# Kernel tuning notes

Hardware: AMD Instinct MI355X
Metric: run time of the kernel (lower is better)

The kernel has to match this reference:

```python
import jax, jax.numpy as jnp
import numpy as np

B, S, E, H, D = 16, 1024, 768, 12, 64  # batch, seq, n_embd, n_head, head_dim
F = 4 * E
EPS = 1e-5


def layernorm(x, g, b):
    mu = jnp.mean(x, axis=-1, keepdims=True)
    var = jnp.mean((x - mu) ** 2, axis=-1, keepdims=True)
    return (x - mu) * jax.lax.rsqrt(var + EPS) * g + b


def setup_inputs() -> dict:
    key = jax.random.key(0)
    ks = jax.random.split(key, 12)
    w = lambda k, shape: jax.random.normal(k, shape, dtype=jnp.float32) * 0.02
    return {
        "x": jax.random.normal(ks[0], (B, S, E), dtype=jnp.float32),
        # per-head q/k/v projections stacked over heads: [H, E, D]
        "Wq": w(ks[1], (H, E, D)), "bq": jnp.zeros((H, D), jnp.float32),
        "Wk": w(ks[2], (H, E, D)), "bk": jnp.zeros((H, D), jnp.float32),
        "Wv": w(ks[3], (H, E, D)), "bv": jnp.zeros((H, D), jnp.float32),
        "Wp": w(ks[4], (E, E)), "bp": jnp.zeros((E,), jnp.float32),
        "ln1_g": jnp.ones((E,), jnp.float32), "ln1_b": jnp.zeros((E,), jnp.float32),
        "ln2_g": jnp.ones((E,), jnp.float32), "ln2_b": jnp.zeros((E,), jnp.float32),
        "W1": w(ks[5], (E, F)), "b1": jnp.zeros((F,), jnp.float32),
        "W2": w(ks[6], (F, E)), "b2": jnp.zeros((E,), jnp.float32),
        "lnf_g": jnp.ones((E,), jnp.float32), "lnf_b": jnp.zeros((E,), jnp.float32),
    }


def reference(x, Wq, bq, Wk, bk, Wv, bv, Wp, bp,
              ln1_g, ln1_b, ln2_g, ln2_b, W1, b1, W2, b2, lnf_g, lnf_b):
    # --- multi-head causal attention (batched over heads, same math as the
    # per-head loop in the original) ---
    h = layernorm(x, ln1_g, ln1_b)
    q = jnp.einsum('bse,hed->bhsd', h, Wq) + bq[None, :, None, :]
    k = jnp.einsum('bse,hed->bhsd', h, Wk) + bk[None, :, None, :]
    v = jnp.einsum('bse,hed->bhsd', h, Wv) + bv[None, :, None, :]
    scores = jnp.einsum('bhsd,bhtd->bhst', q, k)
    causal = jnp.tril(jnp.ones((S, S), dtype=bool))
    # original: mask with -inf, then divide by sqrt(head_dim), then softmax
    scores = jnp.where(causal, scores, -jnp.inf) / np.sqrt(D).astype(np.float32)
    attn = jax.nn.softmax(scores, axis=-1)
    o = jnp.einsum('bhst,bhtd->bhsd', attn, v)
    o = o.transpose(0, 2, 1, 3).reshape(B, S, E)  # concat heads
    x = x + (o @ Wp + bp)
    # --- FFN with post-net LayerNorm (as in the original FeedForward) ---
    h2 = layernorm(x, ln2_g, ln2_b)
    f = jax.nn.gelu(h2 @ W1 + b1, approximate=False) @ W2 + b2
    f = layernorm(f, lnf_g, lnf_b)
    return x + f
```

## Files before the change

kernel.cpp:

```cpp
#include <hip/hip_runtime.h>
#include <math.h>

typedef unsigned short u16;
typedef __attribute__((ext_vector_type(8))) short s16x8;
typedef __attribute__((ext_vector_type(4))) float f32x4;

#define NB 16
#define NS 1024
#define NE 768
#define NH 12
#define ND 64
#define NF 3072
#define NBS (NB*NS)
#define NBH (NB*NH)

__device__ __forceinline__ u16 f2bf(float f){
  unsigned u = __float_as_uint(f);
  unsigned r = (u + 0x7fffu + ((u >> 16) & 1u)) >> 16;
  return (u16)r;
}

__device__ __forceinline__ void gload16(const void* g, void* l){
  __builtin_amdgcn_global_load_lds((const __attribute__((address_space(1))) void*)g,
                                   (__attribute__((address_space(3))) void*)l, 16, 0, 0);
}

__global__ __launch_bounds__(256) void pack_t(const float* __restrict__ W,
                                              u16* __restrict__ Wt, int N, int K){
  __shared__ u16 tile[64*72];
  const int tid = threadIdx.x;
  const int n0 = blockIdx.x*64, k0 = blockIdx.y*64;
  #pragma unroll
  for (int it = 0; it < 4; ++it){
    int c = it*256 + tid;
    int row = c >> 4, col = (c & 15) * 4;
    float4 v = *(const float4*)(W + (size_t)(k0+row)*N + n0 + col);
    tile[row*72+col+0] = f2bf(v.x); tile[row*72+col+1] = f2bf(v.y);
    tile[row*72+col+2] = f2bf(v.z); tile[row*72+col+3] = f2bf(v.w);
  }
  __syncthreads();
  #pragma unroll
  for (int it = 0; it < 2; ++it){
    int c = it*256 + tid;
    int nr = c >> 3, kc = (c & 7) * 8;
    s16x8 val;
    #pragma unroll
    for (int j = 0; j < 8; ++j) val[j] = tile[(kc+j)*72 + nr];
    *(s16x8*)(Wt + (size_t)(n0+nr)*K + k0 + kc) = val;
  }
}

__global__ __launch_bounds__(256) void pack_qkv(const float* __restrict__ Wq,
    const float* __restrict__ Wk, const float* __restrict__ Wv,
    const float* __restrict__ bq, const float* __restrict__ bk,
    const float* __restrict__ bv, u16* __restrict__ Wt, float* __restrict__ bias){
  __shared__ u16 tile[64*72];
  const int tid = threadIdx.x;
  const int n0 = blockIdx.x*64, e0 = blockIdx.y*64;
  const int p = n0 / NE, rr = n0 % NE, h = rr >> 6;
  const float* Wsrc = (p==0) ? Wq : ((p==1) ? Wk : Wv);
  #pragma unroll
  for (int it = 0; it < 4; ++it){
    int c = it*256 + tid;
    int row = c >> 4, col = (c & 15) * 4;
    float4 v = *(const float4*)(Wsrc + ((size_t)h*NE + e0 + row)*ND + col);
    tile[row*72+col+0] = f2bf(v.x); tile[row*72+col+1] = f2bf(v.y);
    tile[row*72+col+2] = f2bf(v.z); tile[row*72+col+3] = f2bf(v.w);
  }
  __syncthreads();
  #pragma unroll
  for (int it = 0; it < 2; ++it){
    int c = it*256 + tid;
    int dr = c >> 3, ec = (c & 7) * 8;
    s16x8 val;
    #pragma unroll
    for (int j = 0; j < 8; ++j) val[j] = tile[(ec+j)*72 + dr];
    *(s16x8*)(Wt + (size_t)(n0+dr)*NE + e0 + ec) = val;
  }
  if (e0 == 0 && tid < 64){
    const float* bsrc = (p==0) ? bq : ((p==1) ? bk : bv);
    bias[n0 + tid] = bsrc[rr + tid];
  }
}

__global__ __launch_bounds__(256) void ln_bf16(const float* __restrict__ x,
    const float* __restrict__ g, const float* __restrict__ b, u16* __restrict__ out){
  __shared__ float red[4];
  const int row = blockIdx.x, tid = threadIdx.x;
  const float* xr = x + (size_t)row*NE;
  float v0 = xr[tid], v1 = xr[tid+256], v2 = xr[tid+512];
  float s = v0 + v1 + v2;
  #pragma unroll
  for (int off = 32; off > 0; off >>= 1) s += __shfl_down(s, off);
  if ((tid & 63) == 0) red[tid >> 6] = s;
  __syncthreads();
  float mu = (red[0]+red[1]+red[2]+red[3]) * (1.f/NE);
  float d0 = v0-mu, d1 = v1-mu, d2 = v2-mu;
  float q = d0*d0 + d1*d1 + d2*d2;
  #pragma unroll
  for (int off = 32; off > 0; off >>= 1) q += __shfl_down(q, off);
  __syncthreads();
  if ((tid & 63) == 0) red[tid >> 6] = q;
  __syncthreads();
  float rs = rsqrtf((red[0]+red[1]+red[2]+red[3]) * (1.f/NE) + 1e-5f);
  u16* orow = out + (size_t)row*NE;
  orow[tid]     = f2bf(d0*rs*g[tid]     + b[tid]);
  orow[tid+256] = f2bf(d1*rs*g[tid+256] + b[tid+256]);
  orow[tid+512] = f2bf(d2*rs*g[tid+512] + b[tid+512]);
}

__global__ __launch_bounds__(256) void ln_add_out(const float* __restrict__ f2,
    const float* __restrict__ g, const float* __restrict__ b, float* __restrict__ x1){
  __shared__ float red[4];
  const int row = blockIdx.x, tid = threadIdx.x;
  const float* xr = f2 + (size_t)row*NE;
  float v0 = xr[tid], v1 = xr[tid+256], v2 = xr[tid+512];
  float s = v0 + v1 + v2;
  #pragma unroll
  for (int off = 32; off > 0; off >>= 1) s += __shfl_down(s, off);
  if ((tid & 63) == 0) red[tid >> 6] = s;
  __syncthreads();
  float mu = (red[0]+red[1]+red[2]+red[3]) * (1.f/NE);
  float d0 = v0-mu, d1 = v1-mu, d2 = v2-mu;
  float q = d0*d0 + d1*d1 + d2*d2;
  #pragma unroll
  for (int off = 32; off > 0; off >>= 1) q += __shfl_down(q, off);
  __syncthreads();
  if ((tid & 63) == 0) red[tid >> 6] = q;
  __syncthreads();
  float rs = rsqrtf((red[0]+red[1]+red[2]+red[3]) * (1.f/NE) + 1e-5f);
  float* orow = x1 + (size_t)row*NE;
  orow[tid]     += d0*rs*g[tid]     + b[tid];
  orow[tid+256] += d1*rs*g[tid+256] + b[tid+256];
  orow[tid+512] += d2*rs*g[tid+512] + b[tid+512];
}

template<int EPI>
__global__ __launch_bounds__(256, 2)
void gemm_bt(const u16* __restrict__ A, const u16* __restrict__ Bt,
             const float* __restrict__ bias, const float* __restrict__ resid,
             float* __restrict__ outF, u16* __restrict__ outU,
             u16* __restrict__ oq, u16* __restrict__ ok, u16* __restrict__ ov,
             int M, int N, int K)
{
  __shared__ u16 As[128*32];
  __shared__ u16 Bs[128*32];
  const int tid = threadIdx.x;
  const int lane = tid & 63, wv = tid >> 6;
  const int wm = wv >> 1, wn = wv & 1;
  const int r = lane & 15, g4 = lane >> 4;
  const int m0 = blockIdx.y*128, n0 = blockIdx.x*128;

  f32x4 acc[4][4] = {};

  for (int kt = 0; kt < K; kt += 32) {
    __syncthreads();
    #pragma unroll
    for (int it = 0; it < 2; ++it) {
      int c = it*256 + tid;
      int row = c >> 2, kc = (c & 3) << 3;
      gload16(A  + (size_t)(m0+row)*K + kt + kc, As + (size_t)(it*256 + wv*64)*8);
      gload16(Bt + (size_t)(n0+row)*K + kt + kc, Bs + (size_t)(it*256 + wv*64)*8);
    }
    __syncthreads();
    s16x8 aF[4], bF[4];
    #pragma unroll
    for (int mi = 0; mi < 4; ++mi)
      aF[mi] = *(const s16x8*)(As + (wm*64 + mi*16 + r)*32 + g4*8);
    #pragma unroll
    for (int ni = 0; ni < 4; ++ni)
      bF[ni] = *(const s16x8*)(Bs + (wn*64 + ni*16 + r)*32 + g4*8);
    #pragma unroll
    for (int mi = 0; mi < 4; ++mi)
      #pragma unroll
      for (int ni = 0; ni < 4; ++ni)
        acc[mi][ni] = __builtin_amdgcn_mfma_f32_16x16x32_bf16(aF[mi], bF[ni], acc[mi][ni], 0, 0, 0);
  }

  const int colb = n0 + wn*64, rowb = m0 + wm*64;
  #pragma unroll
  for (int mi = 0; mi < 4; ++mi) {
    #pragma unroll
    for (int ni = 0; ni < 4; ++ni) {
      const int col = colb + ni*16 + r;
      const float bv = bias[col];
      #pragma unroll
      for (int i = 0; i < 4; ++i) {
        const int row = rowb + mi*16 + g4*4 + i;
        float v = acc[mi][ni][i] + bv;
        if (EPI == 0) {
          int p = col / NE, rr2 = col % NE;
          int hh = rr2 >> 6, d = rr2 & 63;
          int bb = row >> 10, ss = row & (NS-1);
          size_t idx = (((size_t)(bb*NH + hh))*NS + ss)*ND + d;
          u16 val = f2bf(v);
          if (p == 0) oq[idx] = val;
          else if (p == 1) ok[idx] = val;
          else ov[idx] = val;
        } else if (EPI == 1) {
          size_t idx = (size_t)row*NE + col;
          outF[idx] = resid[idx] + v;
        } else if (EPI == 2) {
          float ge = 0.5f * v * (1.0f + erff(v * 0.70710678118654752f));
          outU[(size_t)row*NF + col] = f2bf(ge);
        } else {
          outF[(size_t)row*NE + col] = v;
        }
      }
    }
  }
}

__global__ __launch_bounds__(256) void transpose_v(const u16* __restrict__ v,
                                                   u16* __restrict__ vT){
  __shared__ u16 tile[64*80];
  const int tid = threadIdx.x;
  const int t0 = blockIdx.x*64, bh = blockIdx.y;
  const u16* src = v + ((size_t)bh*NS + t0)*ND;
  #pragma unroll
  for (int it = 0; it < 2; ++it){
    int c = it*256 + tid;
    int row = c >> 3, col = (c & 7) * 8;
    *(s16x8*)(tile + row*80 + col) = *(const s16x8*)(src + (size_t)row*ND + col);
  }
  __syncthreads();
  u16* dst = vT + (size_t)bh*ND*NS + t0;
  #pragma unroll
  for (int it = 0; it < 2; ++it){
    int c = it*256 + tid;
    int d = c >> 3, tc = (c & 7) * 8;
    s16x8 val;
    #pragma unroll
    for (int j = 0; j < 8; ++j) val[j] = tile[(tc+j)*80 + d];
    *(s16x8*)(dst + (size_t)d*NS + tc) = val;
  }
}

__global__ __launch_bounds__(256, 2)
void attn(const u16* __restrict__ q, const u16* __restrict__ k,
          const u16* __restrict__ vT, u16* __restrict__ o)
{
  __shared__ u16 Ks[64*80];
  __shared__ u16 Vs[64*80];
  __shared__ u16 Ps[64*80];
  const int tid = threadIdx.x, lane = tid & 63, w = tid >> 6;
  const int r = lane & 15, g4 = lane >> 4;
  const int qt = blockIdx.x, bh = blockIdx.y;
  const int qs0 = qt*64;
  const int bb = bh / NH, hh = bh % NH;

  const u16* qrow = q + ((size_t)bh*NS + qs0 + w*16 + r)*ND;
  s16x8 qf0 = *(const s16x8*)(qrow + g4*8);
  s16x8 qf1 = *(const s16x8*)(qrow + 32 + g4*8);

  f32x4 oacc[4] = {};
  float mrow[4], lrow[4];
  #pragma unroll
  for (int i = 0; i < 4; ++i){ mrow[i] = -INFINITY; lrow[i] = 0.f; }

  const u16* kbase = k  + (size_t)bh*NS*ND;
  const u16* vbase = vT + (size_t)bh*ND*NS;

  for (int kt0 = 0; kt0 <= qs0; kt0 += 64) {
    __syncthreads();
    #pragma unroll
    for (int it = 0; it < 2; ++it) {
      int c = it*256 + tid;
      int rowi = c >> 3, coli = (c & 7) * 8;
      *(s16x8*)(Ks + rowi*80 + coli) = *(const s16x8*)(kbase + (size_t)(kt0+rowi)*ND + coli);
      *(s16x8*)(Vs + rowi*80 + coli) = *(const s16x8*)(vbase + (size_t)rowi*NS + kt0 + coli);
    }
    __syncthreads();

    f32x4 sc[4];
    #pragma unroll
    for (int ni = 0; ni < 4; ++ni) {
      s16x8 kf0 = *(const s16x8*)(Ks + (ni*16+r)*80 + g4*8);
      s16x8 kf1 = *(const s16x8*)(Ks + (ni*16+r)*80 + 32 + g4*8);
      f32x4 t = {};
      t = __builtin_amdgcn_mfma_f32_16x16x32_bf16(qf0, kf0, t, 0, 0, 0);
      t = __builtin_amdgcn_mfma_f32_16x16x32_bf16(qf1, kf1, t, 0, 0, 0);
      sc[ni] = t;
    }
    const bool diag = (kt0 == qs0);
    float mx[4];
    #pragma unroll
    for (int i = 0; i < 4; ++i) mx[i] = -INFINITY;
    #pragma unroll
    for (int ni = 0; ni < 4; ++ni)
      #pragma unroll
      for (int i = 0; i < 4; ++i) {
        float v = sc[ni][i] * 0.125f;
        if (diag && (kt0 + ni*16 + r > qs0 + w*16 + g4*4 + i)) v = -INFINITY;
        sc[ni][i] = v;
        mx[i] = fmaxf(mx[i], v);
      }
    #pragma unroll
    for (int i = 0; i < 4; ++i) {
      #pragma unroll
      for (int off = 1; off < 16; off <<= 1) mx[i] = fmaxf(mx[i], __shfl_xor(mx[i], off));
    }
    float corr[4], psum[4];
    #pragma unroll
    for (int i = 0; i < 4; ++i) {
      float mn = fmaxf(mrow[i], mx[i]);
      corr[i] = __expf(mrow[i] - mn);
      mrow[i] = mn;
      psum[i] = 0.f;
    }
    #pragma unroll
    for (int ni = 0; ni < 4; ++ni)
      #pragma unroll
      for (int i = 0; i < 4; ++i) {
        float p = __expf(sc[ni][i] - mrow[i]);
        psum[i] += p;
        Ps[(w*16 + g4*4 + i)*80 + ni*16 + r] = f2bf(p);
      }
    #pragma unroll
    for (int i = 0; i < 4; ++i) {
      #pragma unroll
      for (int off = 1; off < 16; off <<= 1) psum[i] += __shfl_xor(psum[i], off);
      lrow[i] = lrow[i]*corr[i] + psum[i];
    }
    #pragma unroll
    for (int di = 0; di < 4; ++di)
      #pragma unroll
      for (int i = 0; i < 4; ++i) oacc[di][i] *= corr[i];
    #pragma unroll
    for (int kk = 0; kk < 2; ++kk) {
      s16x8 pf = *(const s16x8*)(Ps + (w*16 + r)*80 + kk*32 + g4*8);
      #pragma unroll
      for (int di = 0; di < 4; ++di) {
        s16x8 vf = *(const s16x8*)(Vs + (di*16+r)*80 + kk*32 + g4*8);
        oacc[di] = __builtin_amdgcn_mfma_f32_16x16x32_bf16(pf, vf, oacc[di], 0, 0, 0);
      }
    }
  }

  #pragma unroll
  for (int i = 0; i < 4; ++i) {
    float inv = 1.f / lrow[i];
    int s = qs0 + w*16 + g4*4 + i;
    u16* orow = o + ((size_t)(bb*NS + s))*NE + hh*ND;
    #pragma unroll
    for (int di = 0; di < 4; ++di)
      orow[di*16 + r] = f2bf(oacc[di][i] * inv);
  }
}

extern "C" void kernel_launch(void* const* d_in, const int* in_sizes, int n_in,
                              void* d_out, int out_size, void* d_ws, size_t ws_size,
                              hipStream_t stream)
{
  const float* x   = (const float*)d_in[0];
  const float* Wq  = (const float*)d_in[1];
  const float* bq  = (const float*)d_in[2];
  const float* Wk  = (const float*)d_in[3];
  const float* bk  = (const float*)d_in[4];
  const float* Wv  = (const float*)d_in[5];
  const float* bv  = (const float*)d_in[6];
  const float* Wp  = (const float*)d_in[7];
  const float* bp  = (const float*)d_in[8];
  const float* g1  = (const float*)d_in[9];
  const float* b1n = (const float*)d_in[10];
  const float* g2  = (const float*)d_in[11];
  const float* b2n = (const float*)d_in[12];
  const float* W1  = (const float*)d_in[13];
  const float* b1f = (const float*)d_in[14];
  const float* W2  = (const float*)d_in[15];
  const float* b2f = (const float*)d_in[16];
  const float* gf  = (const float*)d_in[17];
  const float* bf  = (const float*)d_in[18];

  char* ws = (char*)d_ws;
  u16*   WqkvT = (u16*)(ws + 0);
  u16*   WpT   = (u16*)(ws + 3538944);
  u16*   W1T   = (u16*)(ws + 4718592);
  u16*   W2T   = (u16*)(ws + 9437184);
  float* qkvb  = (float*)(ws + 14155776);
  u16*   hbuf  = (u16*)(ws + 14164992);
  u16*   qbuf  = (u16*)(ws + 39330816);
  u16*   kbuf  = (u16*)(ws + 64496640);
  u16*   vbuf  = (u16*)(ws + 89662464);
  u16*   vTbuf = (u16*)(ws + 114828288);
  const size_t base_end = 139994112;
  float* f2    = (float*)kbuf;
  float* x1    = (float*)d_out;

  const size_t f1_full = (size_t)NBS * NF * 2;
  u16* f1buf;
  int mc;
  if (ws_size >= base_end + f1_full) {
    f1buf = (u16*)(ws + base_end);
    mc = NBS;
  } else {
    f1buf = vbuf;
    size_t cap = (ws_size < base_end ? ws_size : base_end) - 89662464;
    mc = (int)(cap / ((size_t)NF * 2)) / 128 * 128;
    if (mc <= 0) mc = 128;
    if (mc > NBS) mc = NBS;
  }

  pack_qkv<<<dim3(36, 12), 256, 0, stream>>>(Wq, Wk, Wv, bq, bk, bv, WqkvT, qkvb);
  pack_t  <<<dim3(NE/64, NE/64), 256, 0, stream>>>(Wp, WpT, NE, NE);
  pack_t  <<<dim3(NF/64, NE/64), 256, 0, stream>>>(W1, W1T, NF, NE);
  pack_t  <<<dim3(NE/64, NF/64), 256, 0, stream>>>(W2, W2T, NE, NF);

  ln_bf16<<<NBS, 256, 0, stream>>>(x, g1, b1n, hbuf);
  gemm_bt<0><<<dim3(2304/128, NBS/128), 256, 0, stream>>>(hbuf, WqkvT, qkvb, nullptr,
      nullptr, nullptr, qbuf, kbuf, vbuf, NBS, 2304, NE);
  transpose_v<<<dim3(NS/64, NBH), 256, 0, stream>>>(vbuf, vTbuf);
  attn<<<dim3(NS/64, NBH), 256, 0, stream>>>(qbuf, kbuf, vTbuf, hbuf);
  gemm_bt<1><<<dim3(NE/128, NBS/128), 256, 0, stream>>>(hbuf, WpT, bp, x,
      x1, nullptr, nullptr, nullptr, nullptr, NBS, NE, NE);
  ln_bf16<<<NBS, 256, 0, stream>>>(x1, g2, b2n, qbuf);
  for (int r0 = 0; r0 < NBS; r0 += mc) {
    int m = (NBS - r0 < mc) ? (NBS - r0) : mc;
    gemm_bt<2><<<dim3(NF/128, m/128), 256, 0, stream>>>(qbuf + (size_t)r0*NE, W1T, b1f,
        nullptr, nullptr, f1buf, nullptr, nullptr, nullptr, m, NF, NE);
    gemm_bt<3><<<dim3(NE/128, m/128), 256, 0, stream>>>(f1buf, W2T, b2f, nullptr,
        f2 + (size_t)r0*NE, nullptr, nullptr, nullptr, nullptr, m, NE, NF);
  }
  ln_add_out<<<NBS, 256, 0, stream>>>(f2, gf, bf, x1);
}
```

Before: 724.0 us.

## Double-buffer K/V tiles with register prefetch in causal attention kernel

The attention loop now prefetches the next K/V tile from global memory into registers while the current tile is being computed. It stores the prefetched data into one of two alternating LDS buffers, so one barrier per iteration replaces two. LDS row padding also changes from 80 to 72 elements, and s_setprio raises wave priority around the MFMA sections. This is meant to hide global load latency behind compute, at the cost of more registers and LDS and a possible change in bank-conflict behaviour.

```diff
diff --git a/kernel.cpp b/kernel.cpp
--- a/kernel.cpp
+++ b/kernel.cpp
@@ -236,13 +236,25 @@
   }
 }
 
+__device__ __forceinline__ void load_kv(const u16* __restrict__ kbase,
+                                        const u16* __restrict__ vbase,
+                                        int kt0, int tid, s16x8* kr, s16x8* vr){
+  #pragma unroll
+  for (int it = 0; it < 2; ++it){
+    int c = it*256 + tid;
+    int rowi = c >> 3, coli = (c & 7) * 8;
+    kr[it] = *(const s16x8*)(kbase + (size_t)(kt0+rowi)*ND + coli);
+    vr[it] = *(const s16x8*)(vbase + (size_t)rowi*NS + kt0 + coli);
+  }
+}
+
 __global__ __launch_bounds__(256, 2)
 void attn(const u16* __restrict__ q, const u16* __restrict__ k,
           const u16* __restrict__ vT, u16* __restrict__ o)
 {
-  __shared__ u16 Ks[64*80];
-  __shared__ u16 Vs[64*80];
-  __shared__ u16 Ps[64*80];
+  __shared__ u16 Ks[2][64*72];
+  __shared__ u16 Vs[2][64*72];
+  __shared__ u16 Ps[64*72];
   const int tid = threadIdx.x, lane = tid & 63, w = tid >> 6;
   const int r = lane & 15, g4 = lane >> 4;
   const int qt = blockIdx.x, bh = blockIdx.y;
@@ -260,28 +272,37 @@
 
   const u16* kbase = k  + (size_t)bh*NS*ND;
   const u16* vbase = vT + (size_t)bh*ND*NS;
-
-  for (int kt0 = 0; kt0 <= qs0; kt0 += 64) {
-    __syncthreads();
-    #pragma unroll
-    for (int it = 0; it < 2; ++it) {
+  const int nt = qs0/64 + 1;
+
+  s16x8 kr[2], vr[2];
+  load_kv(kbase, vbase, 0, tid, kr, vr);
+
+  int cur = 0;
+  for (int t = 0; t < nt; ++t) {
+    const int kt0 = t*64;
+    #pragma unroll
+    for (int it = 0; it < 2; ++it){
       int c = it*256 + tid;
       int rowi = c >> 3, coli = (c & 7) * 8;
-      *(s16x8*)(Ks + rowi*80 + coli) = *(const s16x8*)(kbase + (size_t)(kt0+rowi)*ND + coli);
-      *(s16x8*)(Vs + rowi*80 + coli) = *(const s16x8*)(vbase + (size_t)rowi*NS + kt0 + coli);
+      *(s16x8*)(&Ks[cur][rowi*72 + coli]) = kr[it];
+      *(s16x8*)(&Vs[cur][rowi*72 + coli]) = vr[it];
     }
     __syncthreads();
+    if (t+1 < nt) load_kv(kbase, vbase, kt0+64, tid, kr, vr);
 
     f32x4 sc[4];
+    __builtin_amdgcn_s_setprio(1);
     #pragma unroll
     for (int ni = 0; ni < 4; ++ni) {
-      s16x8 kf0 = *(const s16x8*)(Ks + (ni*16+r)*80 + g4*8);
-      s16x8 kf1 = *(const s16x8*)(Ks + (ni*16+r)*80 + 32 + g4*8);
-      f32x4 t = {};
-      t = __builtin_amdgcn_mfma_f32_16x16x32_bf16(qf0, kf0, t, 0, 0, 0);
-      t = __builtin_amdgcn_mfma_f32_16x16x32_bf16(qf1, kf1, t, 0, 0, 0);
-      sc[ni] = t;
-    }
+      s16x8 kf0 = *(const s16x8*)(&Ks[cur][(ni*16+r)*72 + g4*8]);
+      s16x8 kf1 = *(const s16x8*)(&Ks[cur][(ni*16+r)*72 + 32 + g4*8]);
+      f32x4 tacc = {};
+      tacc = __builtin_amdgcn_mfma_f32_16x16x32_bf16(qf0, kf0, tacc, 0, 0, 0);
+      tacc = __builtin_amdgcn_mfma_f32_16x16x32_bf16(qf1, kf1, tacc, 0, 0, 0);
+      sc[ni] = tacc;
+    }
+    __builtin_amdgcn_s_setprio(0);
+
     const bool diag = (kt0 == qs0);
     float mx[4];
     #pragma unroll
@@ -314,7 +335,7 @@
       for (int i = 0; i < 4; ++i) {
         float p = __expf(sc[ni][i] - mrow[i]);
         psum[i] += p;
-        Ps[(w*16 + g4*4 + i)*80 + ni*16 + r] = f2bf(p);
+        Ps[(w*16 + g4*4 + i)*72 + ni*16 + r] = f2bf(p);
       }
     #pragma unroll
     for (int i = 0; i < 4; ++i) {
@@ -326,15 +347,18 @@
     for (int di = 0; di < 4; ++di)
       #pragma unroll
       for (int i = 0; i < 4; ++i) oacc[di][i] *= corr[i];
+    __builtin_amdgcn_s_setprio(1);
     #pragma unroll
     for (int kk = 0; kk < 2; ++kk) {
-      s16x8 pf = *(const s16x8*)(Ps + (w*16 + r)*80 + kk*32 + g4*8);
+      s16x8 pf = *(const s16x8*)(&Ps[(w*16 + r)*72 + kk*32 + g4*8]);
       #pragma unroll
       for (int di = 0; di < 4; ++di) {
-        s16x8 vf = *(const s16x8*)(Vs + (di*16+r)*80 + kk*32 + g4*8);
+        s16x8 vf = *(const s16x8*)(&Vs[cur][(di*16+r)*72 + kk*32 + g4*8]);
         oacc[di] = __builtin_amdgcn_mfma_f32_16x16x32_bf16(pf, vf, oacc[di], 0, 0, 0);
       }
     }
+    __builtin_amdgcn_s_setprio(0);
+    cur ^= 1;
   }
 
   #pragma unroll
```

Result: no change. 727.3 us (+0.5%).

## Process two query tiles per attention block and fold softmax scale into K

Applied to the files above, without the earlier changes.

Each attention workgroup now handles 128 query rows as two 64-row groups that share every loaded K/V tile, halving K/V staging per query and launching half as many blocks. The 1/sqrt(D)*log2(e) factor is folded into K in the QKV GEMM epilogue so softmax can use exp2 without a per-score multiply. Blocks are remapped so neighbouring physical blocks come from different heads, and s_setprio raises wave priority around the MFMA sections. Costs are more registers per thread, which may lower occupancy, and extra K rounding in bf16 after scaling.

```diff
diff --git a/kernel.cpp b/kernel.cpp
--- a/kernel.cpp
+++ b/kernel.cpp
@@ -193,6 +193,7 @@
           int hh = rr2 >> 6, d = rr2 & 63;
           int bb = row >> 10, ss = row & (NS-1);
           size_t idx = (((size_t)(bb*NH + hh))*NS + ss)*ND + d;
+          if (p == 1) v *= 0.18033688011112042f;
           u16 val = f2bf(v);
           if (p == 0) oq[idx] = val;
           else if (p == 1) ok[idx] = val;
@@ -245,23 +246,34 @@
   __shared__ u16 Ps[64*80];
   const int tid = threadIdx.x, lane = tid & 63, w = tid >> 6;
   const int r = lane & 15, g4 = lane >> 4;
-  const int qt = blockIdx.x, bh = blockIdx.y;
-  const int qs0 = qt*64;
+  const int phys = blockIdx.y * 8 + blockIdx.x;
+  const int logical = (phys & 7) * 192 + (phys >> 3);
+  const int bh = logical >> 3, qt = logical & 7;
+  const int qs0 = qt * 128;
   const int bb = bh / NH, hh = bh % NH;
 
-  const u16* qrow = q + ((size_t)bh*NS + qs0 + w*16 + r)*ND;
-  s16x8 qf0 = *(const s16x8*)(qrow + g4*8);
-  s16x8 qf1 = *(const s16x8*)(qrow + 32 + g4*8);
-
-  f32x4 oacc[4] = {};
-  float mrow[4], lrow[4];
-  #pragma unroll
-  for (int i = 0; i < 4; ++i){ mrow[i] = -INFINITY; lrow[i] = 0.f; }
+  s16x8 qf[2][2];
+  {
+    const u16* qb = q + ((size_t)bh*NS + qs0 + w*16 + r)*ND;
+    qf[0][0] = *(const s16x8*)(qb + g4*8);
+    qf[0][1] = *(const s16x8*)(qb + 32 + g4*8);
+    qf[1][0] = *(const s16x8*)(qb + (size_t)64*ND + g4*8);
+    qf[1][1] = *(const s16x8*)(qb + (size_t)64*ND + 32 + g4*8);
+  }
+
+  f32x4 oacc[2][4] = {};
+  float mrow[2][4], lrow[2][4];
+  #pragma unroll
+  for (int rg = 0; rg < 2; ++rg)
+    #pragma unroll
+    for (int i = 0; i < 4; ++i){ mrow[rg][i] = -INFINITY; lrow[rg][i] = 0.f; }
 
   const u16* kbase = k  + (size_t)bh*NS*ND;
   const u16* vbase = vT + (size_t)bh*ND*NS;
-
-  for (int kt0 = 0; kt0 <= qs0; kt0 += 64) {
+  const int nt = qs0/64 + 2;
+
+  for (int t = 0; t < nt; ++t) {
+    const int kt0 = t*64;
     __syncthreads();
     #pragma unroll
     for (int it = 0; it < 2; ++it) {
@@ -272,80 +284,96 @@
     }
     __syncthreads();
 
-    f32x4 sc[4];
-    #pragma unroll
-    for (int ni = 0; ni < 4; ++ni) {
-      s16x8 kf0 = *(const s16x8*)(Ks + (ni*16+r)*80 + g4*8);
-      s16x8 kf1 = *(const s16x8*)(Ks + (ni*16+r)*80 + 32 + g4*8);
-      f32x4 t = {};
-      t = __builtin_amdgcn_mfma_f32_16x16x32_bf16(qf0, kf0, t, 0, 0, 0);
-      t = __builtin_amdgcn_mfma_f32_16x16x32_bf16(qf1, kf1, t, 0, 0, 0);
-      sc[ni] = t;
+    #pragma unroll
+    for (int rg = 0; rg < 2; ++rg) {
+      const int rgb = qs0 + rg*64;
+      if (kt0 > rgb) continue;
+
+      f32x4 sc[4];
+      __builtin_amdgcn_s_setprio(1);
+      #pragma unroll
+      for (int ni = 0; ni < 4; ++ni) {
+        s16x8 kf0 = *(const s16x8*)(Ks + (ni*16+r)*80 + g4*8);
+        s16x8 kf1 = *(const s16x8*)(Ks + (ni*16+r)*80 + 32 + g4*8);
+        f32x4 tacc = {};
+        tacc = __builtin_amdgcn_mfma_f32_16x16x32_bf16(qf[rg][0], kf0, tacc, 0, 0, 0);
+        tacc = __builtin_amdgcn_mfma_f32_16x16x32_bf16(qf[rg][1], kf1, tacc, 0, 0, 0);
+        sc[ni] = tacc;
+      }
+      __builtin_amdgcn_s_setprio(0);
+
+      float mx[4];
+      #pragma unroll
+      for (int i = 0; i < 4; ++i) mx[i] = mrow[rg][i];
+      if (kt0 == rgb) {
+        #pragma unroll
+        for (int ni = 0; ni < 4; ++ni)
+          #pragma unroll
+          for (int i = 0; i < 4; ++i) {
+            if (ni*16 + r > w*16 + g4*4 + i) sc[ni][i] = -INFINITY;
+            mx[i] = fmaxf(mx[i], sc[ni][i]);
+          }
+      } else {
+        #pragma unroll
+        for (int ni = 0; ni < 4; ++ni)
+          #pragma unroll
+          for (int i = 0; i < 4; ++i) mx[i] = fmaxf(mx[i], sc[ni][i]);
+      }
+      #pragma unroll
+      for (int i = 0; i < 4; ++i) {
+        #pragma unroll
+        for (int off = 1; off < 16; off <<= 1) mx[i] = fmaxf(mx[i], __shfl_xor(mx[i], off));
+      }
+      float corr[4], psum[4];
+      #pragma unroll
+      for (int i = 0; i < 4; ++i) {
+        corr[i] = exp2f(mrow[rg][i] - mx[i]);
+        mrow[rg][i] = mx[i];
+        psum[i] = 0.f;
+      }
+      #pragma unroll
+      for (int ni = 0; ni < 4; ++ni)
+        #pragma unroll
+        for (int i = 0; i < 4; ++i) {
+          float p = exp2f(sc[ni][i] - mrow[rg][i]);
+          psum[i] += p;
+          Ps[(w*16 + g4*4 + i)*80 + ni*16 + r] = f2bf(p);
+        }
+      #pragma unroll
+      for (int i = 0; i < 4; ++i) {
+        #pragma unroll
+        for (int off = 1; off < 16; off <<= 1) psum[i] += __shfl_xor(psum[i], off);
+        lrow[rg][i] = lrow[rg][i]*corr[i] + psum[i];
+      }
+      #pragma unroll
+      for (int di = 0; di < 4; ++di)
+        #pragma unroll
+        for (int i = 0; i < 4; ++i) oacc[rg][di][i] *= corr[i];
+      __builtin_amdgcn_s_setprio(1);
+      #pragma unroll
+      for (int kk = 0; kk < 2; ++kk) {
+        s16x8 pf = *(const s16x8*)(Ps + (w*16 + r)*80 + kk*32 + g4*8);
+        #pragma unroll
+        for (int di = 0; di < 4; ++di) {
+          s16x8 vf = *(const s16x8*)(Vs + (di*16+r)*80 + kk*32 + g4*8);
+          oacc[rg][di] = __builtin_amdgcn_mfma_f32_16x16x32_bf16(pf, vf, oacc[rg][di], 0, 0, 0);
+        }
+      }
+      __builtin_amdgcn_s_setprio(0);
     }
-    const bool diag = (kt0 == qs0);
-    float mx[4];
-    #pragma unroll
-    for (int i = 0; i < 4; ++i) mx[i] = -INFINITY;
-    #pragma unroll
-    for (int ni = 0; ni < 4; ++ni)
-      #pragma unroll
-      for (int i = 0; i < 4; ++i) {
-        float v = sc[ni][i] * 0.125f;
-        if (diag && (kt0 + ni*16 + r > qs0 + w*16 + g4*4 + i)) v = -INFINITY;
-        sc[ni][i] = v;
-        mx[i] = fmaxf(mx[i], v);
-      }
+  }
+
+  #pragma unroll
+  for (int rg = 0; rg < 2; ++rg)
     #pragma unroll
     for (int i = 0; i < 4; ++i) {
-      #pragma unroll
-      for (int off = 1; off < 16; off <<= 1) mx[i] = fmaxf(mx[i], __shfl_xor(mx[i], off));
+      float inv = 1.f / lrow[rg][i];
+      int s = qs0 + rg*64 + w*16 + g4*4 + i;
+      u16* orow = o + ((size_t)(bb*NS + s))*NE + hh*ND;
+      #pragma unroll
+      for (int di = 0; di < 4; ++di)
+        orow[di*16 + r] = f2bf(oacc[rg][di][i] * inv);
     }
-    float corr[4], psum[4];
-    #pragma unroll
-    for (int i = 0; i < 4; ++i) {
-      float mn = fmaxf(mrow[i], mx[i]);
-      corr[i] = __expf(mrow[i] - mn);
-      mrow[i] = mn;
-      psum[i] = 0.f;
-    }
-    #pragma unroll
-    for (int ni = 0; ni < 4; ++ni)
-      #pragma unroll
-      for (int i = 0; i < 4; ++i) {
-        float p = __expf(sc[ni][i] - mrow[i]);
-        psum[i] += p;
-        Ps[(w*16 + g4*4 + i)*80 + ni*16 + r] = f2bf(p);
-      }
-    #pragma unroll
-    for (int i = 0; i < 4; ++i) {
-      #pragma unroll
-      for (int off = 1; off < 16; off <<= 1) psum[i] += __shfl_xor(psum[i], off);
-      lrow[i] = lrow[i]*corr[i] + psum[i];
-    }
-    #pragma unroll
-    for (int di = 0; di < 4; ++di)
-      #pragma unroll
-      for (int i = 0; i < 4; ++i) oacc[di][i] *= corr[i];
-    #pragma unroll
-    for (int kk = 0; kk < 2; ++kk) {
-      s16x8 pf = *(const s16x8*)(Ps + (w*16 + r)*80 + kk*32 + g4*8);
-      #pragma unroll
-      for (int di = 0; di < 4; ++di) {
-        s16x8 vf = *(const s16x8*)(Vs + (di*16+r)*80 + kk*32 + g4*8);
-        oacc[di] = __builtin_amdgcn_mfma_f32_16x16x32_bf16(pf, vf, oacc[di], 0, 0, 0);
-      }
-    }
-  }
-
-  #pragma unroll
-  for (int i = 0; i < 4; ++i) {
-    float inv = 1.f / lrow[i];
-    int s = qs0 + w*16 + g4*4 + i;
-    u16* orow = o + ((size_t)(bb*NS + s))*NE + hh*ND;
-    #pragma unroll
-    for (int di = 0; di < 4; ++di)
-      orow[di*16 + r] = f2bf(oacc[di][i] * inv);
-  }
 }
 
 extern "C" void kernel_launch(void* const* d_in, const int* in_sizes, int n_in,
@@ -410,7 +438,7 @@
   gemm_bt<0><<<dim3(2304/128, NBS/128), 256, 0, stream>>>(hbuf, WqkvT, qkvb, nullptr,
       nullptr, nullptr, qbuf, kbuf, vbuf, NBS, 2304, NE);
   transpose_v<<<dim3(NS/64, NBH), 256, 0, stream>>>(vbuf, vTbuf);
-  attn<<<dim3(NS/64, NBH), 256, 0, stream>>>(qbuf, kbuf, vTbuf, hbuf);
+  attn<<<dim3(NS/128, NBH), 256, 0, stream>>>(qbuf, kbuf, vTbuf, hbuf);
   gemm_bt<1><<<dim3(NE/128, NBS/128), 256, 0, stream>>>(hbuf, WpT, bp, x,
       x1, nullptr, nullptr, nullptr, nullptr, NBS, NE, NE);
   ln_bf16<<<NBS, 256, 0, stream>>>(x1, g2, b2n, qbuf);
```

Measured after the change: 707.5 us. -2.3%, faster.
